# Kernel tuning notes

Measured on AMD Instinct MI355X. Metric: run time of the kernel, lower is better.

## Reference

```python
import jax, jax.numpy as jnp
import numpy as np

B, T, F = 200, 250, 14
H, D, C = 256, 164, 8


def _lstm(x, W, U, b):
    """Keras-semantics LSTM. x: [B,T,F_in]. Returns (all_h [B,T,H], last_h [B,H]).
    Gate order i, f, c(g), o; sigmoid recurrent activations, tanh cell activation."""
    Bx = x.shape[0]
    units = U.shape[0]
    # precompute input projections for all timesteps: [T, B, 4H]
    xz = jnp.einsum('btf,fk->tbk', x, W) + b

    def step(carry, xz_t):
        h, c = carry
        z = xz_t + h @ U
        i, f, g, o = jnp.split(z, 4, axis=-1)
        i = jax.nn.sigmoid(i)
        f = jax.nn.sigmoid(f)
        g = jnp.tanh(g)
        o = jax.nn.sigmoid(o)
        c = f * c + i * g
        h = o * jnp.tanh(c)
        return (h, c), h

    h0 = jnp.zeros((Bx, units), x.dtype)
    (hT, _), hs = jax.lax.scan(step, (h0, h0), xz)
    return jnp.swapaxes(hs, 0, 1), hT


def setup_inputs() -> dict:
    key = jax.random.key(0)
    ks = jax.random.split(key, 8)
    s = 0.05
    return {
        'inputs': jax.random.normal(ks[0], (B, T, F), jnp.float32),
        'W1': jax.random.normal(ks[1], (F, 4 * H), jnp.float32) * s,
        'U1': jax.random.normal(ks[2], (H, 4 * H), jnp.float32) * s,
        'b1': jnp.zeros((4 * H,), jnp.float32),
        'W2': jax.random.normal(ks[3], (H, 4 * H), jnp.float32) * s,
        'U2': jax.random.normal(ks[4], (H, 4 * H), jnp.float32) * s,
        'b2': jnp.zeros((4 * H,), jnp.float32),
        'Wd': jax.random.normal(ks[5], (H, D), jnp.float32) * s,
        'bd': jnp.zeros((D,), jnp.float32),
        'Ws': jax.random.normal(ks[6], (D, C), jnp.float32) * s,
        'bs': jnp.zeros((C,), jnp.float32),
    }


def reference(inputs, W1, U1, b1, W2, U2, b2, Wd, bd, Ws, bs):
    # LSTM 1: return_sequences=True
    seq, _ = _lstm(inputs, W1, U1, b1)          # [B,T,H]
    # LSTM 2: last hidden state only
    _, h2 = _lstm(seq, W2, U2, b2)              # [B,H]
    hidden = jax.nn.relu(h2 @ Wd + bd)          # [B,D]
    probs = jax.nn.softmax(hidden @ Ws + bs, axis=-1)  # [B,C]
    return probs
```

## Files before the change

kernel.cpp:

```cpp
#include <hip/hip_runtime.h>


#define T_STEPS 250
#define B_REAL  200
#define BPAD    208
#define FIN     14
#define HID     256
#define NGATE   1024
#define NBG     13
#define L1S     2
#define L2S     4
#define SLAB    (BPAD*HID)
#define XT_ROW  32
#define XT_ELEMS (T_STEPS*BPAD*XT_ROW)
#define FSTRIDE 32
#define F1N     ((long long)T_STEPS*NBG*FSTRIDE)
#define F2N     ((long long)(T_STEPS+1)*NBG*FSTRIDE)

typedef __bf16 bf16_t;
typedef __bf16 bf16x8 __attribute__((ext_vector_type(8)));
typedef float  f32x4  __attribute__((ext_vector_type(4)));

__device__ __forceinline__ float sigmoid_f(float x) {
  return 1.f / (1.f + __expf(-x));
}
__device__ __forceinline__ float tanh_f(float x) {
  float e = __expf(2.f * x);
  return 1.f - 2.f / (e + 1.f);
}

__device__ __forceinline__ unsigned int ld_flag_sc0(const unsigned int* p) {
  unsigned int v;
  asm volatile("global_load_dword %0, %1, off sc0\n\ts_waitcnt vmcnt(0)"
               : "=v"(v) : "v"(p) : "memory");
  return v;
}
__device__ __forceinline__ unsigned int ld_flag_sc01(const unsigned int* p) {
  unsigned int v;
  asm volatile("global_load_dword %0, %1, off sc0 sc1\n\ts_waitcnt vmcnt(0)"
               : "=v"(v) : "v"(p) : "memory");
  return v;
}
__device__ __forceinline__ void st_flag_sc0(unsigned int* p) {
  unsigned int one = 1u;
  asm volatile("global_store_dword %0, %1, off sc0" :: "v"(p), "v"(one) : "memory");
}
__device__ __forceinline__ void st_flag_sc01(unsigned int* p) {
  unsigned int one = 1u;
  asm volatile("global_store_dword %0, %1, off sc0 sc1" :: "v"(p), "v"(one) : "memory");
}
__device__ __forceinline__ void st_bf16_sc01(bf16_t* p, bf16_t v) {
  unsigned int u = (unsigned int)__builtin_bit_cast(unsigned short, v);
  asm volatile("global_store_short %0, %1, off sc0 sc1" :: "v"(p), "v"(u) : "memory");
}
__device__ __forceinline__ void waitcnt0() {
  asm volatile("s_waitcnt vmcnt(0)" ::: "memory");
}

__device__ __forceinline__ int poll_dual(const unsigned int* fa,
                                         const unsigned int* fb) {
  int it = 0;
  for (;;) {
    if (ld_flag_sc0(fa) != 0u) return 0;
    if ((++it & 15) == 0 && ld_flag_sc01(fb) != 0u) return 1;
  }
}

__device__ __forceinline__ long long fidx(int t, int g, int s) {
  return ((long long)t * NBG + g) * FSTRIDE + s;
}

__global__ void prep_kernel(const float* __restrict__ x,
                            bf16_t* __restrict__ xT,
                            bf16_t* __restrict__ seq,
                            bf16_t* __restrict__ h2seq,
                            unsigned int* __restrict__ fa1,
                            unsigned int* __restrict__ fb1,
                            unsigned int* __restrict__ fa2,
                            unsigned int* __restrict__ fb2)
{
  long long i = (long long)blockIdx.x * blockDim.x + threadIdx.x;
  const long long total = (long long)XT_ELEMS + SLAB + SLAB + 2*F1N + 2*F2N;
  if (i >= total) return;
  if (i < XT_ELEMS) {
    int t  = (int)(i / (BPAD * XT_ROW));
    int r  = (int)(i % (BPAD * XT_ROW));
    int b  = r / XT_ROW, kk = r % XT_ROW;
    float v = 0.f;
    if (b < B_REAL && kk < FIN) v = x[((long long)b * T_STEPS + t) * FIN + kk];
    xT[i] = (bf16_t)v;
    return;
  }
  i -= XT_ELEMS;
  if (i < SLAB) { seq[i] = (bf16_t)0.f; return; }
  i -= SLAB;
  if (i < SLAB) { h2seq[i] = (bf16_t)0.f; return; }
  i -= SLAB;
  if (i < F1N) { fa1[i] = 0u; return; }
  i -= F1N;
  if (i < F1N) { fb1[i] = 0u; return; }
  i -= F1N;
  if (i < F2N) { fa2[i] = 0u; return; }
  i -= F2N;
  fb2[i] = 0u;
}

__global__ __launch_bounds__(512) void lstm_fused(
    const float* __restrict__ W1, const float* __restrict__ U1,
    const float* __restrict__ b1,
    const float* __restrict__ W2, const float* __restrict__ U2,
    const float* __restrict__ b2,
    const bf16_t* __restrict__ xT,
    bf16_t* __restrict__ seq, bf16_t* __restrict__ h2s,
    unsigned int* __restrict__ fa1, unsigned int* __restrict__ fb1,
    unsigned int* __restrict__ fa2, unsigned int* __restrict__ fb2)
{
  __shared__ float zs[4096];
  const int xcd = blockIdx.x & 7;
  const int slot = blockIdx.x >> 3;
  int g, role;
  if (slot < 6)      { g = xcd;     role = slot; }
  else if (xcd < 5)  { g = 8 + xcd; role = slot - 6; }
  else return;

  const int tid = threadIdx.x;
  const int l   = tid & 63;
  const int lr  = l & 15;
  const int ag  = l >> 4;
  const int w   = tid >> 6;
  const int b0  = g * 16;

  if (role < L1S) {
    const int hsl  = role;
    const int unit = hsl * 128 + w * 16 + lr;

    f32x4 wb[4][9];
#pragma unroll
    for (int gg = 0; gg < 4; ++gg) {
      const int n = gg * 256 + unit;
#pragma unroll
      for (int kf = 0; kf < 9; ++kf) {
        bf16x8 v;
#pragma unroll
        for (int e = 0; e < 8; ++e) {
          const int k = kf * 32 + ag * 8 + e;
          float val = 0.f;
          if (k < 256)            val = U1[(long long)k * NGATE + n];
          else if (k - 256 < FIN) val = W1[(long long)(k - 256) * NGATE + n];
          v[e] = (bf16_t)val;
        }
        wb[gg][kf] = __builtin_bit_cast(f32x4, v);
      }
    }
    float bias[4];
#pragma unroll
    for (int gg = 0; gg < 4; ++gg) bias[gg] = b1[gg * 256 + unit];
    float cst[4] = {0.f, 0.f, 0.f, 0.f};

    for (int t = 0; t < T_STEPS; ++t) {
#pragma unroll
      for (int gg = 0; gg < 4; ++gg)
#pragma unroll
        for (int kf = 0; kf < 9; ++kf)
          asm volatile("" : "+v"(wb[gg][kf]));
      if (t > 0) {
        waitcnt0();
        __syncthreads();
        if (tid == 0) st_flag_sc01(fb1 + fidx(t - 1, g, hsl));
        int slow = 0;
        if (l < L1S && l != hsl)
          slow = poll_dual(fa1 + fidx(t - 1, g, l), fb1 + fidx(t - 1, g, l));
        if (__any(slow))
          __builtin_amdgcn_fence(__ATOMIC_ACQUIRE, "agent");
      }

      const bf16_t* arow = seq + (long long)t * SLAB + (b0 + lr) * HID;
      f32x4 acc[4] = {{0.f,0.f,0.f,0.f},{0.f,0.f,0.f,0.f},
                      {0.f,0.f,0.f,0.f},{0.f,0.f,0.f,0.f}};
#pragma unroll
      for (int kf = 0; kf < 8; ++kf) {
        const bf16x8 a = *(const bf16x8*)(arow + kf * 32 + ag * 8);
#pragma unroll
        for (int gg = 0; gg < 4; ++gg)
          acc[gg] = __builtin_amdgcn_mfma_f32_16x16x32_bf16(
              a, __builtin_bit_cast(bf16x8, wb[gg][kf]), acc[gg], 0, 0, 0);
      }
      {
        const bf16x8 ax = *(const bf16x8*)(xT + ((long long)t * BPAD + b0 + lr) * XT_ROW + ag * 8);
#pragma unroll
        for (int gg = 0; gg < 4; ++gg)
          acc[gg] = __builtin_amdgcn_mfma_f32_16x16x32_bf16(
              ax, __builtin_bit_cast(bf16x8, wb[gg][8]), acc[gg], 0, 0, 0);
      }
      bf16_t* orow = seq + (long long)(t + 1) * SLAB;
      bf16_t hv[4];
#pragma unroll
      for (int r = 0; r < 4; ++r) {
        const float ig = sigmoid_f(acc[0][r] + bias[0]);
        const float fg = sigmoid_f(acc[1][r] + bias[1]);
        const float gg = tanh_f  (acc[2][r] + bias[2]);
        const float og = sigmoid_f(acc[3][r] + bias[3]);
        const float c  = fg * cst[r] + ig * gg;
        cst[r] = c;
        hv[r] = (bf16_t)(og * tanh_f(c));
        orow[(b0 + ag * 4 + r) * HID + unit] = hv[r];
      }
      waitcnt0();
      __syncthreads();
      if (tid == 0) st_flag_sc0(fa1 + fidx(t, g, hsl));
#pragma unroll
      for (int r = 0; r < 4; ++r)
        st_bf16_sc01(orow + (b0 + ag * 4 + r) * HID + unit, hv[r]);
    }
    waitcnt0();
    __syncthreads();
    if (tid == 0) st_flag_sc01(fb1 + fidx(T_STEPS - 1, g, hsl));
  } else {
    const int hsl  = role - L1S;
    const int uq   = w & 3;
    const int kh   = w >> 2;
    const int unit = hsl * 64 + uq * 16 + lr;

    const float* Wsrc = kh ? W2 : U2;
    f32x4 wb[4][8];
#pragma unroll
    for (int gg = 0; gg < 4; ++gg) {
      const int n = gg * 256 + unit;
#pragma unroll
      for (int kf = 0; kf < 8; ++kf) {
        bf16x8 v;
#pragma unroll
        for (int e = 0; e < 8; ++e)
          v[e] = (bf16_t)Wsrc[(long long)(kf * 32 + ag * 8 + e) * NGATE + n];
        wb[gg][kf] = __builtin_bit_cast(f32x4, v);
      }
    }
    float bias[4];
#pragma unroll
    for (int gg = 0; gg < 4; ++gg) bias[gg] = b2[gg * 256 + unit];
    float cst[4] = {0.f, 0.f, 0.f, 0.f};

    for (int t = 0; t < T_STEPS; ++t) {
#pragma unroll
      for (int gg = 0; gg < 4; ++gg)
#pragma unroll
        for (int kf = 0; kf < 8; ++kf)
          asm volatile("" : "+v"(wb[gg][kf]));
      waitcnt0();
      __syncthreads();
      if (t > 0 && tid == 0) st_flag_sc01(fb2 + fidx(t, g, hsl));
      int slow = 0;
      if (kh == 1) {
        if (l < L1S)
          slow = poll_dual(fa1 + fidx(t, g, l), fb1 + fidx(t, g, l));
      } else if (t > 0) {
        if (l < L2S && l != hsl)
          slow = poll_dual(fa2 + fidx(t, g, l), fb2 + fidx(t, g, l));
      }
      if (__any(slow))
        __builtin_amdgcn_fence(__ATOMIC_ACQUIRE, "agent");

      const bf16_t* arow = kh
          ? (seq + (long long)(t + 1) * SLAB + (b0 + lr) * HID)
          : (h2s + (long long)t       * SLAB + (b0 + lr) * HID);
      f32x4 acc[4] = {{0.f,0.f,0.f,0.f},{0.f,0.f,0.f,0.f},
                      {0.f,0.f,0.f,0.f},{0.f,0.f,0.f,0.f}};
#pragma unroll
      for (int kf = 0; kf < 8; ++kf) {
        const bf16x8 a = *(const bf16x8*)(arow + kf * 32 + ag * 8);
#pragma unroll
        for (int gg = 0; gg < 4; ++gg)
          acc[gg] = __builtin_amdgcn_mfma_f32_16x16x32_bf16(
              a, __builtin_bit_cast(bf16x8, wb[gg][kf]), acc[gg], 0, 0, 0);
      }
      if (kh == 1) {
#pragma unroll
        for (int gg = 0; gg < 4; ++gg)
#pragma unroll
          for (int r = 0; r < 4; ++r)
            zs[((gg * 4 + uq) * 16 + ag * 4 + r) * 16 + lr] = acc[gg][r];
      }
      __syncthreads();
      bf16_t* orow = h2s + (long long)(t + 1) * SLAB;
      bf16_t hv[4];
      if (kh == 0) {
#pragma unroll
        for (int r = 0; r < 4; ++r) {
          const int row = ag * 4 + r;
          const float zi = acc[0][r] + zs[((0 * 4 + uq) * 16 + row) * 16 + lr] + bias[0];
          const float zf = acc[1][r] + zs[((1 * 4 + uq) * 16 + row) * 16 + lr] + bias[1];
          const float zg = acc[2][r] + zs[((2 * 4 + uq) * 16 + row) * 16 + lr] + bias[2];
          const float zo = acc[3][r] + zs[((3 * 4 + uq) * 16 + row) * 16 + lr] + bias[3];
          const float ig = sigmoid_f(zi);
          const float fg = sigmoid_f(zf);
          const float gg = tanh_f(zg);
          const float og = sigmoid_f(zo);
          const float c  = fg * cst[r] + ig * gg;
          cst[r] = c;
          hv[r] = (bf16_t)(og * tanh_f(c));
          orow[(b0 + row) * HID + unit] = hv[r];
        }
      }
      waitcnt0();
      __syncthreads();
      if (tid == 0) st_flag_sc0(fa2 + fidx(t + 1, g, hsl));
      if (kh == 0) {
#pragma unroll
        for (int r = 0; r < 4; ++r)
          st_bf16_sc01(orow + (b0 + ag * 4 + r) * HID + unit, hv[r]);
      }
    }
    waitcnt0();
    __syncthreads();
    if (tid == 0) st_flag_sc01(fb2 + fidx(T_STEPS, g, hsl));
  }
}

__global__ __launch_bounds__(64) void head_kernel(
    const bf16_t* __restrict__ h2,
    const float* __restrict__ Wd, const float* __restrict__ bd,
    const float* __restrict__ Ws, const float* __restrict__ bs,
    float* __restrict__ out)
{
  __shared__ float hsm[HID];
  __shared__ float hid[164];
  __shared__ float lg[8];
  const int b = blockIdx.x, tid = threadIdx.x;
  const bf16_t* hr = h2 + (long long)b * HID;
  for (int k = tid; k < HID; k += 64) hsm[k] = (float)hr[k];
  __syncthreads();
  for (int d = tid; d < 164; d += 64) {
    float a = bd[d];
    for (int k = 0; k < HID; ++k) a = fmaf(hsm[k], Wd[k * 164 + d], a);
    hid[d] = fmaxf(a, 0.f);
  }
  __syncthreads();
  if (tid < 8) {
    float a = bs[tid];
    for (int k = 0; k < 164; ++k) a = fmaf(hid[k], Ws[k * 8 + tid], a);
    lg[tid] = a;
  }
  __syncthreads();
  if (tid < 8) {
    float m = lg[0];
#pragma unroll
    for (int j = 1; j < 8; ++j) m = fmaxf(m, lg[j]);
    float s = 0.f;
#pragma unroll
    for (int j = 0; j < 8; ++j) s += __expf(lg[j] - m);
    out[b * 8 + tid] = __expf(lg[tid] - m) / s;
  }
}

extern "C" void kernel_launch(void* const* d_in, const int* in_sizes, int n_in,
                              void* d_out, int out_size, void* d_ws, size_t ws_size,
                              hipStream_t stream)
{
  const float* x  = (const float*)d_in[0];
  const float* W1 = (const float*)d_in[1];
  const float* U1 = (const float*)d_in[2];
  const float* b1 = (const float*)d_in[3];
  const float* W2 = (const float*)d_in[4];
  const float* U2 = (const float*)d_in[5];
  const float* b2 = (const float*)d_in[6];
  const float* Wd = (const float*)d_in[7];
  const float* bd = (const float*)d_in[8];
  const float* Ws = (const float*)d_in[9];
  const float* bs = (const float*)d_in[10];
  (void)in_sizes; (void)n_in; (void)out_size; (void)ws_size;

  char* p = (char*)d_ws;
  size_t off = 0;
  auto carve = [&](size_t bytes) -> void* {
    void* r = p + off;
    off = (off + bytes + 255) & ~(size_t)255;
    return r;
  };
  bf16_t* xT  = (bf16_t*)carve((size_t)XT_ELEMS * 2);
  bf16_t* seq = (bf16_t*)carve((size_t)(T_STEPS + 1) * SLAB * 2);
  bf16_t* h2s = (bf16_t*)carve((size_t)(T_STEPS + 1) * SLAB * 2);
  unsigned int* fa1 = (unsigned int*)carve((size_t)F1N * 4);
  unsigned int* fb1 = (unsigned int*)carve((size_t)F1N * 4);
  unsigned int* fa2 = (unsigned int*)carve((size_t)F2N * 4);
  unsigned int* fb2 = (unsigned int*)carve((size_t)F2N * 4);

  const long long prep_total = (long long)XT_ELEMS + SLAB + SLAB + 2*F1N + 2*F2N;
  const int pb = (int)((prep_total + 255) / 256);

  prep_kernel<<<pb, 256, 0, stream>>>(x, xT, seq, h2s, fa1, fb1, fa2, fb2);
  lstm_fused<<<96, 512, 0, stream>>>(W1, U1, b1, W2, U2, b2,
                                     xT, seq, h2s, fa1, fb1, fa2, fb2);
  head_kernel<<<B_REAL, 64, 0, stream>>>(h2s + (long long)T_STEPS * SLAB,
                                         Wd, bd, Ws, bs, (float*)d_out);
}
```

Baseline: 1.294 ms.

## Replace block barriers with per-wave flags and double-buffered shared exchange

```diff
diff --git a/kernel.cpp b/kernel.cpp
--- a/kernel.cpp
+++ b/kernel.cpp
@@ -14,6 +14,7 @@
 #define XT_ROW  32
 #define XT_ELEMS (T_STEPS*BPAD*XT_ROW)
 #define FSTRIDE 32
+#define NF      16
 #define F1N     ((long long)T_STEPS*NBG*FSTRIDE)
 #define F2N     ((long long)(T_STEPS+1)*NBG*FSTRIDE)
 
@@ -41,46 +42,42 @@
                : "=v"(v) : "v"(p) : "memory");
   return v;
 }
-__device__ __forceinline__ void st_flag_sc0(unsigned int* p) {
-  unsigned int one = 1u;
-  asm volatile("global_store_dword %0, %1, off sc0" :: "v"(p), "v"(one) : "memory");
-}
 __device__ __forceinline__ void st_flag_sc01(unsigned int* p) {
   unsigned int one = 1u;
-  asm volatile("global_store_dword %0, %1, off sc0 sc1" :: "v"(p), "v"(one) : "memory");
+  asm volatile("global_store_dword %0, %1, off sc0 sc1" :: "v"(p), "v"(one));
 }
 __device__ __forceinline__ void st_bf16_sc01(bf16_t* p, bf16_t v) {
   unsigned int u = (unsigned int)__builtin_bit_cast(unsigned short, v);
-  asm volatile("global_store_short %0, %1, off sc0 sc1" :: "v"(p), "v"(u) : "memory");
+  asm volatile("global_store_short %0, %1, off sc0 sc1" :: "v"(p), "v"(u));
 }
 __device__ __forceinline__ void waitcnt0() {
-  asm volatile("s_waitcnt vmcnt(0)" ::: "memory");
-}
-
-__device__ __forceinline__ int poll_dual(const unsigned int* fa,
-                                         const unsigned int* fb) {
+  asm volatile("s_waitcnt vmcnt(0)");
+}
+
+__device__ __forceinline__ void poll_flags(const unsigned int* rec, int l) {
   int it = 0;
   for (;;) {
-    if (ld_flag_sc0(fa) != 0u) return 0;
-    if ((++it & 15) == 0 && ld_flag_sc01(fb) != 0u) return 1;
-  }
-}
-
-__device__ __forceinline__ long long fidx(int t, int g, int s) {
-  return ((long long)t * NBG + g) * FSTRIDE + s;
+    unsigned int v = 1u;
+    if (l < NF)
+      v = ((it & 7) == 7) ? ld_flag_sc01(rec + l) : ld_flag_sc0(rec + l);
+    if (__all(v != 0u)) return;
+    ++it;
+  }
+}
+
+__device__ __forceinline__ long long fidx(int t, int g) {
+  return ((long long)t * NBG + g) * FSTRIDE;
 }
 
 __global__ void prep_kernel(const float* __restrict__ x,
                             bf16_t* __restrict__ xT,
                             bf16_t* __restrict__ seq,
                             bf16_t* __restrict__ h2seq,
-                            unsigned int* __restrict__ fa1,
-                            unsigned int* __restrict__ fb1,
-                            unsigned int* __restrict__ fa2,
-                            unsigned int* __restrict__ fb2)
+                            unsigned int* __restrict__ f1,
+                            unsigned int* __restrict__ f2)
 {
   long long i = (long long)blockIdx.x * blockDim.x + threadIdx.x;
-  const long long total = (long long)XT_ELEMS + SLAB + SLAB + 2*F1N + 2*F2N;
+  const long long total = (long long)XT_ELEMS + SLAB + SLAB + F1N + F2N;
   if (i >= total) return;
   if (i < XT_ELEMS) {
     int t  = (int)(i / (BPAD * XT_ROW));
@@ -96,26 +93,23 @@
   i -= SLAB;
   if (i < SLAB) { h2seq[i] = (bf16_t)0.f; return; }
   i -= SLAB;
-  if (i < F1N) { fa1[i] = 0u; return; }
+  if (i < F1N) { f1[i] = 0u; return; }
   i -= F1N;
-  if (i < F1N) { fb1[i] = 0u; return; }
-  i -= F1N;
-  if (i < F2N) { fa2[i] = 0u; return; }
-  i -= F2N;
-  fb2[i] = 0u;
-}
-
-__global__ __launch_bounds__(512) void lstm_fused(
+  f2[i] = 0u;
+}
+
+__global__ __launch_bounds__(512)
+__attribute__((amdgpu_waves_per_eu(2, 2)))
+void lstm_fused(
     const float* __restrict__ W1, const float* __restrict__ U1,
     const float* __restrict__ b1,
     const float* __restrict__ W2, const float* __restrict__ U2,
     const float* __restrict__ b2,
     const bf16_t* __restrict__ xT,
     bf16_t* __restrict__ seq, bf16_t* __restrict__ h2s,
-    unsigned int* __restrict__ fa1, unsigned int* __restrict__ fb1,
-    unsigned int* __restrict__ fa2, unsigned int* __restrict__ fb2)
+    unsigned int* __restrict__ f1, unsigned int* __restrict__ f2)
 {
-  __shared__ float zs[4096];
+  __shared__ float zs[2][4096];
   const int xcd = blockIdx.x & 7;
   const int slot = blockIdx.x >> 3;
   int g, role;
@@ -131,8 +125,9 @@
   const int b0  = g * 16;
 
   if (role < L1S) {
-    const int hsl  = role;
-    const int unit = hsl * 128 + w * 16 + lr;
+    const int hsl    = role;
+    const int unit   = hsl * 128 + w * 16 + lr;
+    const int myslot = hsl * 8 + w;
 
     f32x4 wb[4][9];
 #pragma unroll
@@ -152,9 +147,8 @@
         wb[gg][kf] = __builtin_bit_cast(f32x4, v);
       }
     }
-    float bias[4];
-#pragma unroll
-    for (int gg = 0; gg < 4; ++gg) bias[gg] = b1[gg * 256 + unit];
+    f32x4 bv = { b1[0 * 256 + unit], b1[1 * 256 + unit],
+                 b1[2 * 256 + unit], b1[3 * 256 + unit] };
     float cst[4] = {0.f, 0.f, 0.f, 0.f};
 
     for (int t = 0; t < T_STEPS; ++t) {
@@ -163,16 +157,9 @@
 #pragma unroll
         for (int kf = 0; kf < 9; ++kf)
           asm volatile("" : "+v"(wb[gg][kf]));
-      if (t > 0) {
-        waitcnt0();
-        __syncthreads();
-        if (tid == 0) st_flag_sc01(fb1 + fidx(t - 1, g, hsl));
-        int slow = 0;
-        if (l < L1S && l != hsl)
-          slow = poll_dual(fa1 + fidx(t - 1, g, l), fb1 + fidx(t - 1, g, l));
-        if (__any(slow))
-          __builtin_amdgcn_fence(__ATOMIC_ACQUIRE, "agent");
-      }
+      asm volatile("" : "+v"(bv));
+
+      if (t > 0) poll_flags(f1 + fidx(t - 1, g), l);
 
       const bf16_t* arow = seq + (long long)t * SLAB + (b0 + lr) * HID;
       f32x4 acc[4] = {{0.f,0.f,0.f,0.f},{0.f,0.f,0.f,0.f},
@@ -193,33 +180,26 @@
               ax, __builtin_bit_cast(bf16x8, wb[gg][8]), acc[gg], 0, 0, 0);
       }
       bf16_t* orow = seq + (long long)(t + 1) * SLAB;
-      bf16_t hv[4];
 #pragma unroll
       for (int r = 0; r < 4; ++r) {
-        const float ig = sigmoid_f(acc[0][r] + bias[0]);
-        const float fg = sigmoid_f(acc[1][r] + bias[1]);
-        const float gg = tanh_f  (acc[2][r] + bias[2]);
-        const float og = sigmoid_f(acc[3][r] + bias[3]);
+        const float ig = sigmoid_f(acc[0][r] + bv[0]);
+        const float fg = sigmoid_f(acc[1][r] + bv[1]);
+        const float gg = tanh_f  (acc[2][r] + bv[2]);
+        const float og = sigmoid_f(acc[3][r] + bv[3]);
         const float c  = fg * cst[r] + ig * gg;
         cst[r] = c;
-        hv[r] = (bf16_t)(og * tanh_f(c));
-        orow[(b0 + ag * 4 + r) * HID + unit] = hv[r];
+        st_bf16_sc01(orow + (b0 + ag * 4 + r) * HID + unit,
+                     (bf16_t)(og * tanh_f(c)));
       }
       waitcnt0();
-      __syncthreads();
-      if (tid == 0) st_flag_sc0(fa1 + fidx(t, g, hsl));
-#pragma unroll
-      for (int r = 0; r < 4; ++r)
-        st_bf16_sc01(orow + (b0 + ag * 4 + r) * HID + unit, hv[r]);
+      if (l == 0) st_flag_sc01(f1 + fidx(t, g) + myslot);
     }
-    waitcnt0();
-    __syncthreads();
-    if (tid == 0) st_flag_sc01(fb1 + fidx(T_STEPS - 1, g, hsl));
   } else {
-    const int hsl  = role - L1S;
-    const int uq   = w & 3;
-    const int kh   = w >> 2;
-    const int unit = hsl * 64 + uq * 16 + lr;
+    const int hsl    = role - L1S;
+    const int uq     = w & 3;
+    const int kh     = w >> 2;
+    const int unit   = hsl * 64 + uq * 16 + lr;
+    const int myslot = hsl * 4 + uq;
 
     const float* Wsrc = kh ? W2 : U2;
     f32x4 wb[4][8];
@@ -235,9 +215,8 @@
         wb[gg][kf] = __builtin_bit_cast(f32x4, v);
       }
     }
-    float bias[4];
-#pragma unroll
-    for (int gg = 0; gg < 4; ++gg) bias[gg] = b2[gg * 256 + unit];
+    f32x4 bv = { b2[0 * 256 + unit], b2[1 * 256 + unit],
+                 b2[2 * 256 + unit], b2[3 * 256 + unit] };
     float cst[4] = {0.f, 0.f, 0.f, 0.f};
 
     for (int t = 0; t < T_STEPS; ++t) {
@@ -246,19 +225,10 @@
 #pragma unroll
         for (int kf = 0; kf < 8; ++kf)
           asm volatile("" : "+v"(wb[gg][kf]));
-      waitcnt0();
-      __syncthreads();
-      if (t > 0 && tid == 0) st_flag_sc01(fb2 + fidx(t, g, hsl));
-      int slow = 0;
-      if (kh == 1) {
-        if (l < L1S)
-          slow = poll_dual(fa1 + fidx(t, g, l), fb1 + fidx(t, g, l));
-      } else if (t > 0) {
-        if (l < L2S && l != hsl)
-          slow = poll_dual(fa2 + fidx(t, g, l), fb2 + fidx(t, g, l));
-      }
-      if (__any(slow))
-        __builtin_amdgcn_fence(__ATOMIC_ACQUIRE, "agent");
+      asm volatile("" : "+v"(bv));
+
+      if (kh == 1)      poll_flags(f1 + fidx(t, g), l);
+      else if (t > 0)   poll_flags(f2 + fidx(t, g), l);
 
       const bf16_t* arow = kh
           ? (seq + (long long)(t + 1) * SLAB + (b0 + lr) * HID)
@@ -274,45 +244,37 @@
               a, __builtin_bit_cast(bf16x8, wb[gg][kf]), acc[gg], 0, 0, 0);
       }
       if (kh == 1) {
+        float* z = zs[t & 1];
 #pragma unroll
         for (int gg = 0; gg < 4; ++gg)
 #pragma unroll
           for (int r = 0; r < 4; ++r)
-            zs[((gg * 4 + uq) * 16 + ag * 4 + r) * 16 + lr] = acc[gg][r];
+            z[((gg * 4 + uq) * 16 + ag * 4 + r) * 16 + lr] = acc[gg][r];
       }
       __syncthreads();
-      bf16_t* orow = h2s + (long long)(t + 1) * SLAB;
-      bf16_t hv[4];
       if (kh == 0) {
+        const float* z = zs[t & 1];
+        bf16_t* orow = h2s + (long long)(t + 1) * SLAB;
 #pragma unroll
         for (int r = 0; r < 4; ++r) {
           const int row = ag * 4 + r;
-          const float zi = acc[0][r] + zs[((0 * 4 + uq) * 16 + row) * 16 + lr] + bias[0];
-          const float zf = acc[1][r] + zs[((1 * 4 + uq) * 16 + row) * 16 + lr] + bias[1];
-          const float zg = acc[2][r] + zs[((2 * 4 + uq) * 16 + row) * 16 + lr] + bias[2];
-          const float zo = acc[3][r] + zs[((3 * 4 + uq) * 16 + row) * 16 + lr] + bias[3];
+          const float zi = acc[0][r] + z[((0 * 4 + uq) * 16 + row) * 16 + lr] + bv[0];
+          const float zf = acc[1][r] + z[((1 * 4 + uq) * 16 + row) * 16 + lr] + bv[1];
+          const float zg = acc[2][r] + z[((2 * 4 + uq) * 16 + row) * 16 + lr] + bv[2];
+          const float zo = acc[3][r] + z[((3 * 4 + uq) * 16 + row) * 16 + lr] + bv[3];
           const float ig = sigmoid_f(zi);
           const float fg = sigmoid_f(zf);
           const float gg = tanh_f(zg);
           const float og = sigmoid_f(zo);
           const float c  = fg * cst[r] + ig * gg;
           cst[r] = c;
-          hv[r] = (bf16_t)(og * tanh_f(c));
-          orow[(b0 + row) * HID + unit] = hv[r];
+          st_bf16_sc01(orow + (b0 + row) * HID + unit,
+                       (bf16_t)(og * tanh_f(c)));
         }
-      }
-      waitcnt0();
-      __syncthreads();
-      if (tid == 0) st_flag_sc0(fa2 + fidx(t + 1, g, hsl));
-      if (kh == 0) {
-#pragma unroll
-        for (int r = 0; r < 4; ++r)
-          st_bf16_sc01(orow + (b0 + ag * 4 + r) * HID + unit, hv[r]);
+        waitcnt0();
+        if (l == 0) st_flag_sc01(f2 + fidx(t + 1, g) + myslot);
       }
     }
-    waitcnt0();
-    __syncthreads();
-    if (tid == 0) st_flag_sc01(fb2 + fidx(T_STEPS, g, hsl));
   }
 }
 
@@ -379,17 +341,15 @@
   bf16_t* xT  = (bf16_t*)carve((size_t)XT_ELEMS * 2);
   bf16_t* seq = (bf16_t*)carve((size_t)(T_STEPS + 1) * SLAB * 2);
   bf16_t* h2s = (bf16_t*)carve((size_t)(T_STEPS + 1) * SLAB * 2);
-  unsigned int* fa1 = (unsigned int*)carve((size_t)F1N * 4);
-  unsigned int* fb1 = (unsigned int*)carve((size_t)F1N * 4);
-  unsigned int* fa2 = (unsigned int*)carve((size_t)F2N * 4);
-  unsigned int* fb2 = (unsigned int*)carve((size_t)F2N * 4);
-
-  const long long prep_total = (long long)XT_ELEMS + SLAB + SLAB + 2*F1N + 2*F2N;
+  unsigned int* f1 = (unsigned int*)carve((size_t)F1N * 4);
+  unsigned int* f2 = (unsigned int*)carve((size_t)F2N * 4);
+
+  const long long prep_total = (long long)XT_ELEMS + SLAB + SLAB + F1N + F2N;
   const int pb = (int)((prep_total + 255) / 256);
 
-  prep_kernel<<<pb, 256, 0, stream>>>(x, xT, seq, h2s, fa1, fb1, fa2, fb2);
+  prep_kernel<<<pb, 256, 0, stream>>>(x, xT, seq, h2s, f1, f2);
   lstm_fused<<<96, 512, 0, stream>>>(W1, U1, b1, W2, U2, b2,
-                                     xT, seq, h2s, fa1, fb1, fa2, fb2);
+                                     xT, seq, h2s, f1, f2);
   head_kernel<<<B_REAL, 64, 0, stream>>>(h2s + (long long)T_STEPS * SLAB,
                                          Wd, bd, Ws, bs, (float*)d_out);
 }
```

Result: slower. 1.328 ms (+2.6%).
